# Performance work log

Measured on AMD Instinct MI355X. Metric: run time of the kernel, lower is better.

The kernel has to match this reference:

```python
import jax, jax.numpy as jnp
import numpy as np

B, S, E = 4, 2048, 1024

def setup_inputs() -> dict:
    key = jax.random.key(0)
    ks = jax.random.split(key, 9)
    lim = 1.0 / np.sqrt(E)
    inp = {
        "query": jax.random.normal(ks[0], (B, S, E), dtype=jnp.float32),
        "key": jax.random.normal(ks[1], (B, S, E), dtype=jnp.float32),
        "value": jax.random.normal(ks[2], (B, S, E), dtype=jnp.float32),
        "Wq": jax.random.uniform(ks[3], (E, E), jnp.float32, -lim, lim),
        "bq": jax.random.uniform(ks[4], (E,), jnp.float32, -lim, lim),
        "Wk": jax.random.uniform(ks[5], (E, E), jnp.float32, -lim, lim),
        "bk": jax.random.uniform(ks[6], (E,), jnp.float32, -lim, lim),
        "Wv": jax.random.uniform(ks[7], (E, E), jnp.float32, -lim, lim),
        "bv": jax.random.uniform(ks[8], (E,), jnp.float32, -lim, lim),
    }
    return inp

def reference(query, key, value, Wq, bq, Wk, bk, Wv, bv):
    # Linear layers (torch stores weight as [out,in]; here W is [in,out] used as x @ W)
    q = query @ Wq + bq            # [B,S,E]
    k = key @ Wk + bk              # [B,S,E]
    v = value @ Wv + bv            # [B,S,E]
    inv_scale = jnp.asarray(E, q.dtype) ** 0.5
    scores = jnp.einsum("bse,bte->bst", q, k) / inv_scale  # [B,S,S]
    attn = jax.nn.softmax(scores, axis=-1)
    # dropout_p = 0.0 -> identity
    out = jnp.einsum("bst,bte->bse", attn, v)  # [B,S,E]
    return out
```

## Files before the change

### kernel.cpp

```cpp
#include <hip/hip_runtime.h>
#include <hip/hip_bf16.h>


typedef __bf16 bf16_t;
typedef bf16_t bf16x8 __attribute__((ext_vector_type(8)));
typedef bf16_t bf16x4 __attribute__((ext_vector_type(4)));
typedef float  f32x4  __attribute__((ext_vector_type(4)));

typedef const __attribute__((address_space(1))) unsigned gl_uint;
typedef __attribute__((address_space(3))) unsigned lds_uint;

#define BM 128
#define BN 128
#define BK 64

__device__ __forceinline__ void gload_lds16(const void* g, void* l) {
  __builtin_amdgcn_global_load_lds((gl_uint*)g, (lds_uint*)l, 16, 0, 0);
}

#define VMCNT(N) asm volatile("s_waitcnt vmcnt(" #N ")" ::: "memory")
#define LGKM0()  asm volatile("s_waitcnt lgkmcnt(0)" ::: "memory")

__device__ __forceinline__ void gemm_v3(
    const bf16_t* __restrict__ Ab, const bf16_t* __restrict__ Bb,
    bf16_t* Lb, f32x4 acc[4][4])
{
  const int tid  = threadIdx.x;
  const int lane = tid & 63;
  const int l15  = lane & 15;
  const int quad = lane >> 4;
  const int wid  = tid >> 6;
  const int wr   = wid >> 1;
  const int wcl  = wid & 1;
  const int swz0 = (quad ^ (l15 & 7)) * 8;
  const int swz1 = ((quad + 4) ^ (l15 & 7)) * 8;

  const int r8 = tid >> 3, s8 = tid & 7;
  const size_t gbase = (size_t)r8 * 1024 + (size_t)((s8 ^ (r8 & 7)) * 8);
  const int dbase = tid * 8;

#define SLOTA(s) (Lb + (s) * 24576)
#define SLOTB(s) (Lb + (s) * 24576 + 16384)
#define STAGE6(ktile, slot) { \
    const bf16_t* _A = Ab + (size_t)(ktile) * 64; \
    const bf16_t* _B = Bb + (size_t)(ktile) * 64; \
    bf16_t* _la = SLOTA(slot); bf16_t* _lb = SLOTB(slot); \
    gload_lds16(_A + gbase,                     _la + dbase); \
    gload_lds16(_A + gbase + (size_t)64 * 1024, _la + dbase + 4096); \
    gload_lds16(_A + gbase + (size_t)128 * 1024, _la + dbase + 8192); \
    gload_lds16(_A + gbase + (size_t)192 * 1024, _la + dbase + 12288); \
    gload_lds16(_B + gbase,                     _lb + dbase); \
    gload_lds16(_B + gbase + (size_t)64 * 1024, _lb + dbase + 4096); }

  const int aoff = (wr * 64 + l15) * 64;
  const int boff = (wcl * 64 + l15) * 64;

#define RD(slot, FA, FB) { \
    const bf16_t* _a = SLOTA(slot) + aoff; \
    const bf16_t* _b = SLOTB(slot) + boff; \
    _Pragma("unroll") for (int mi = 0; mi < 4; ++mi) { \
      FA[mi][0] = *(const bf16x8*)(_a + mi * 1024 + swz0); \
      FA[mi][1] = *(const bf16x8*)(_a + mi * 1024 + swz1); } \
    _Pragma("unroll") for (int ni = 0; ni < 4; ++ni) { \
      FB[ni][0] = *(const bf16x8*)(_b + ni * 1024 + swz0); \
      FB[ni][1] = *(const bf16x8*)(_b + ni * 1024 + swz1); } }

#define MFM(FA, FB) \
    _Pragma("unroll") for (int kk = 0; kk < 2; ++kk) \
    _Pragma("unroll") for (int mi = 0; mi < 4; ++mi) \
    _Pragma("unroll") for (int ni = 0; ni < 4; ++ni) \
      acc[mi][ni] = __builtin_amdgcn_mfma_f32_16x16x32_bf16( \
          FA[mi][kk], FB[ni][kk], acc[mi][ni], 0, 0, 0);

  bf16x8 fa0[4][2], fb0[4][2], fa1[4][2], fb1[4][2];

  STAGE6(0, 0); STAGE6(1, 1); STAGE6(2, 2);
  VMCNT(6);
  __builtin_amdgcn_s_barrier();
  RD(0, fa0, fb0);
  LGKM0();
  __builtin_amdgcn_s_barrier();

#pragma unroll
  for (int kt = 0; kt < 14; ++kt) {
    const int ss = kt % 3;
    const int rs = (kt + 1) % 3;
    if (kt <= 12) STAGE6(kt + 3, ss);
    if ((kt & 1) == 0) { RD(rs, fa1, fb1); MFM(fa0, fb0); }
    else               { RD(rs, fa0, fb0); MFM(fa1, fb1); }
    if (kt <= 12) { VMCNT(6); }
    else          { VMCNT(0); }
    __builtin_amdgcn_s_barrier();
  }
  RD(0, fa1, fb1); MFM(fa0, fb0);
  MFM(fa1, fb1);

#undef SLOTA
#undef SLOTB
#undef STAGE6
#undef RD
#undef MFM
}

__global__ __launch_bounds__(512, 2)
void qkv_v3(const bf16_t* __restrict__ qb, const bf16_t* __restrict__ kb,
            const bf16_t* __restrict__ vb, const bf16_t* __restrict__ Wqt,
            const bf16_t* __restrict__ Wkt, const bf16_t* __restrict__ Wvt,
            const float* __restrict__ bq, const float* __restrict__ bk,
            const float* __restrict__ bv, bf16_t* __restrict__ qp,
            bf16_t* __restrict__ kp, bf16_t* __restrict__ vT)
{
  __shared__ __align__(16) bf16_t lds[3 * 24576];
  const int L   = blockIdx.x;
  const int lin = (L & 7) * 96 + (L >> 3);
  const int z   = lin >> 8;
  const int r   = lin & 255;
  const int by  = r >> 3, bx = r & 7;
  const int K = 1024, N = 1024;

  const bf16_t* A    = (z == 0) ? qb : (z == 1) ? kb : vb;
  const bf16_t* W    = (z == 0) ? Wqt : (z == 1) ? Wkt : Wvt;
  const float*  bias = (z == 0) ? bq : (z == 1) ? bk : bv;

  f32x4 acc[4][4];
  const f32x4 z4 = {0.f, 0.f, 0.f, 0.f};
#pragma unroll
  for (int i = 0; i < 4; ++i)
#pragma unroll
    for (int j = 0; j < 4; ++j) acc[i][j] = z4;

  gemm_v3(A + (size_t)by * 256 * K, W + (size_t)bx * 128 * K, lds, acc);

  const int tid = threadIdx.x;
  const int lane = tid & 63, l15 = lane & 15, quad = lane >> 4;
  const int wid = tid >> 6, wr = wid >> 1, wcl = wid & 1;
  const int m0 = by * 256 + wr * 64;
  const int n0 = bx * 128 + wcl * 64;
  float bv_[4];
#pragma unroll
  for (int ni = 0; ni < 4; ++ni) bv_[ni] = bias[n0 + ni * 16 + l15];

  if (z < 2) {
    bf16_t* C = (z == 0) ? qp : kp;
#pragma unroll
    for (int mi = 0; mi < 4; ++mi) {
      const int gm = m0 + mi * 16 + quad * 4;
#pragma unroll
      for (int ni = 0; ni < 4; ++ni) {
        const int gn = n0 + ni * 16 + l15;
        f32x4 a = acc[mi][ni];
#pragma unroll
        for (int rr = 0; rr < 4; ++rr)
          C[(size_t)(gm + rr) * N + gn] = (bf16_t)(a[rr] + bv_[ni]);
      }
    }
  } else {
#pragma unroll
    for (int mi = 0; mi < 4; ++mi) {
      const int gm = m0 + mi * 16 + quad * 4;
      const int b = gm >> 11;
      const int s = gm & 2047;
#pragma unroll
      for (int ni = 0; ni < 4; ++ni) {
        const int gn = n0 + ni * 16 + l15;
        f32x4 a = acc[mi][ni];
        bf16x4 o;
#pragma unroll
        for (int rr = 0; rr < 4; ++rr) o[rr] = (bf16_t)(a[rr] + bv_[ni]);
        *(bf16x4*)&vT[((size_t)b * N + gn) * 2048 + s] = o;
      }
    }
  }
}

__global__ __launch_bounds__(512, 2)
void scores_v3(const bf16_t* __restrict__ qp, const bf16_t* __restrict__ kp,
               bf16_t* __restrict__ P)
{
  __shared__ __align__(16) bf16_t lds[3 * 24576];
  const int L   = blockIdx.x;
  const int lin = (L & 7) * 64 + (L >> 3);
  const int bz  = lin >> 7;
  const int r   = lin & 127;
  const int by  = r >> 4, bx = r & 15;
  const int K = 1024;

  const bf16_t* Ab = qp + (size_t)bz * 2048 * 1024 + (size_t)by * 256 * K;
  const bf16_t* Bb = kp + (size_t)bz * 2048 * 1024 + (size_t)bx * 128 * K;

  f32x4 acc[4][4];
  const f32x4 z4 = {0.f, 0.f, 0.f, 0.f};
#pragma unroll
  for (int i = 0; i < 4; ++i)
#pragma unroll
    for (int j = 0; j < 4; ++j) acc[i][j] = z4;

  gemm_v3(Ab, Bb, lds, acc);

  const int tid = threadIdx.x;
  const int lane = tid & 63, l15 = lane & 15, quad = lane >> 4;
  const int wid = tid >> 6, wr = wid >> 1, wcl = wid & 1;
  const int m0 = by * 256 + wr * 64;
  const int n0 = bx * 128 + wcl * 64;
  bf16_t* C = P + (size_t)bz * 2048 * 2048;
  const float cexp = 0.03125f * 1.4426950408889634f;
#pragma unroll
  for (int mi = 0; mi < 4; ++mi) {
    const int gm = m0 + mi * 16 + quad * 4;
#pragma unroll
    for (int ni = 0; ni < 4; ++ni) {
      const int gn = n0 + ni * 16 + l15;
      f32x4 a = acc[mi][ni];
#pragma unroll
      for (int rr = 0; rr < 4; ++rr)
        C[(size_t)(gm + rr) * 2048 + gn] = (bf16_t)exp2f(a[rr] * cexp);
    }
  }
}

template <bool LSUM>
__device__ __forceinline__ void mfma_tile(const bf16_t* As, const bf16_t* Bs,
                                          f32x4 acc[4][4], f32x4 acc_l[4]) {
  const int lane = threadIdx.x & 63;
  const int quad = lane >> 4;
  const int l15  = lane & 15;
  const int wid  = threadIdx.x >> 6;
  const int wm   = (wid >> 1) * 64;
  const int wn   = (wid & 1) * 64;
  const int csw  = l15 & 7;
  bf16x8 ones;
  if (LSUM) {
#pragma unroll
    for (int t = 0; t < 8; ++t) ones[t] = (bf16_t)1.0f;
  }
#pragma unroll
  for (int ks = 0; ks < 2; ++ks) {
    const int sg = ks * 4 + quad;
    const int c  = (sg ^ csw) * 8;
    bf16x8 fa[4], fb[4];
#pragma unroll
    for (int i = 0; i < 4; ++i)
      fa[i] = *(const bf16x8*)&As[(wm + i * 16 + l15) * BK + c];
#pragma unroll
    for (int i = 0; i < 4; ++i)
      fb[i] = *(const bf16x8*)&Bs[(wn + i * 16 + l15) * BK + c];
#pragma unroll
    for (int mi = 0; mi < 4; ++mi)
#pragma unroll
      for (int ni = 0; ni < 4; ++ni)
        acc[mi][ni] = __builtin_amdgcn_mfma_f32_16x16x32_bf16(
            fa[mi], fb[ni], acc[mi][ni], 0, 0, 0);
    if (LSUM) {
#pragma unroll
      for (int mi = 0; mi < 4; ++mi)
        acc_l[mi] = __builtin_amdgcn_mfma_f32_16x16x32_bf16(
            fa[mi], ones, acc_l[mi], 0, 0, 0);
    }
  }
}

template <bool LSUM>
__device__ __forceinline__ void gemm_core_bf16(
    const bf16_t* __restrict__ Ab, const bf16_t* __restrict__ Bb,
    const int K, bf16_t* As, bf16_t* Bs, f32x4 acc[4][4], f32x4 acc_l[4])
{
  const int tid = threadIdx.x;
  for (int kt = 0; kt < K; kt += BK) {
#pragma unroll
    for (int j = 0; j < 4; ++j) {
      const int lin = j * 256 + tid;
      const int row = lin >> 3;
      const int seg = (lin & 7) ^ (row & 7);
      gload_lds16(Ab + (size_t)row * K + kt + seg * 8, &As[lin * 8]);
    }
#pragma unroll
    for (int j = 0; j < 4; ++j) {
      const int lin = j * 256 + tid;
      const int row = lin >> 3;
      const int seg = (lin & 7) ^ (row & 7);
      gload_lds16(Bb + (size_t)row * K + kt + seg * 8, &Bs[lin * 8]);
    }
    __syncthreads();
    mfma_tile<LSUM>(As, Bs, acc, acc_l);
    __syncthreads();
  }
}

template <int MODE>
__global__ __launch_bounds__(256, 2)
void gemm_att(const bf16_t* __restrict__ A, const bf16_t* __restrict__ Bt,
              void* __restrict__ Cv,
              const int M, const int N, const int K,
              const long long sA, const long long sB, const long long sC)
{
  __shared__ __align__(16) bf16_t As[BM * BK];
  __shared__ __align__(16) bf16_t Bs[BN * BK];

  const int L = blockIdx.x;
  int bx, by, bz;
  if (MODE == 0) {
    const int g = L >> 3;
    const int gst = (L & 7) * 2 + (g >> 6);
    bz = gst >> 2;
    const int s2 = gst & 3;
    const int w = g & 63;
    bx = (s2 & 1) * 8 + (w & 7);
    by = (s2 >> 1) * 8 + (w >> 3);
  } else {
    const int xcd = L & 7;
    const int w = (L >> 3) & 63;
    bz = xcd >> 1;
    bx = w & 7;
    by = (xcd & 1) * 8 + (w >> 3);
  }

  const bf16_t* Ab = A + (size_t)bz * sA + (size_t)by * BM * K;
  const bf16_t* Bb = Bt + (size_t)bz * sB + (size_t)bx * BN * K;

  f32x4 acc[4][4];
  f32x4 acc_l[4];
  const f32x4 z4 = {0.f, 0.f, 0.f, 0.f};
#pragma unroll
  for (int i = 0; i < 4; ++i) {
    acc_l[i] = z4;
#pragma unroll
    for (int j = 0; j < 4; ++j) acc[i][j] = z4;
  }

  gemm_core_bf16<MODE == 1>(Ab, Bb, K, As, Bs, acc, acc_l);

  const int lane = threadIdx.x & 63;
  const int quad = lane >> 4;
  const int l15  = lane & 15;
  const int wid  = threadIdx.x >> 6;
  const int wm = (wid >> 1) * 64, wn = (wid & 1) * 64;
  const int m0 = by * BM, n0 = bx * BN;

  if (MODE == 0) {
    const float cexp = 0.03125f * 1.4426950408889634f;
    bf16_t* C = (bf16_t*)Cv + (size_t)bz * sC;
#pragma unroll
    for (int mi = 0; mi < 4; ++mi) {
      const int gm = m0 + wm + mi * 16 + quad * 4;
#pragma unroll
      for (int ni = 0; ni < 4; ++ni) {
        const int gn = n0 + wn + ni * 16 + l15;
        f32x4 a = acc[mi][ni];
#pragma unroll
        for (int r = 0; r < 4; ++r)
          C[(size_t)(gm + r) * N + gn] = (bf16_t)exp2f(a[r] * cexp);
      }
    }
  } else {
    float* C = (float*)Cv + (size_t)bz * sC;
#pragma unroll
    for (int mi = 0; mi < 4; ++mi) {
      const int gm = m0 + wm + mi * 16 + quad * 4;
      float il[4];
#pragma unroll
      for (int r = 0; r < 4; ++r) il[r] = 1.0f / acc_l[mi][r];
#pragma unroll
      for (int ni = 0; ni < 4; ++ni) {
        const int gn = n0 + wn + ni * 16 + l15;
        f32x4 a = acc[mi][ni];
#pragma unroll
        for (int r = 0; r < 4; ++r)
          C[(size_t)(gm + r) * N + gn] = a[r] * il[r];
      }
    }
  }
}

__global__ __launch_bounds__(256)
void prep(const float* __restrict__ q, const float* __restrict__ k,
          const float* __restrict__ v, const float* __restrict__ Wq,
          const float* __restrict__ Wk, const float* __restrict__ Wv,
          bf16_t* __restrict__ qo, bf16_t* __restrict__ ko,
          bf16_t* __restrict__ vo, bf16_t* __restrict__ Wqt,
          bf16_t* __restrict__ Wkt, bf16_t* __restrict__ Wvt) {
  const int L = blockIdx.x;
  const int tid = threadIdx.x;
  if (L < 24576) {
    const int z = L >> 13;
    const int blk = L & 8191;
    const float* in = (z == 0) ? q : (z == 1) ? k : v;
    bf16_t* out = (z == 0) ? qo : (z == 1) ? ko : vo;
    const size_t i = ((size_t)blk * 256 + tid) * 4;
    const float4 w = *(const float4*)(in + i);
    bf16x4 o;
    o[0] = (bf16_t)w.x; o[1] = (bf16_t)w.y; o[2] = (bf16_t)w.z; o[3] = (bf16_t)w.w;
    *(bf16x4*)(out + i) = o;
  } else {
    const int t = L - 24576;
    const int z = t >> 8;
    const int wi = t & 255;
    const float* W = (z == 0) ? Wq : (z == 1) ? Wk : Wv;
    bf16_t* Wt = (z == 0) ? Wqt : (z == 1) ? Wkt : Wvt;
    __shared__ float tile[64][65];
    const int n0 = (wi & 15) * 64;
    const int k0 = (wi >> 4) * 64;
#pragma unroll
    for (int it = 0; it < 16; ++it) {
      const int idx = it * 256 + tid;
      const int r = idx >> 6, c = idx & 63;
      tile[r][c] = W[(size_t)(k0 + r) * 1024 + n0 + c];
    }
    __syncthreads();
#pragma unroll
    for (int it = 0; it < 16; ++it) {
      const int idx = it * 256 + tid;
      const int r = idx >> 6, c = idx & 63;
      Wt[(size_t)(n0 + r) * 1024 + k0 + c] = (bf16_t)tile[c][r];
    }
  }
}

extern "C" void kernel_launch(void* const* d_in, const int* in_sizes, int n_in,
                              void* d_out, int out_size, void* d_ws, size_t ws_size,
                              hipStream_t stream) {
  const int B = 4, S = 2048, E = 1024;
  const size_t BSE = (size_t)B * S * E;
  const size_t EE  = (size_t)E * E;

  const float* q_in = (const float*)d_in[0];
  const float* k_in = (const float*)d_in[1];
  const float* v_in = (const float*)d_in[2];
  const float* Wq = (const float*)d_in[3];
  const float* bq = (const float*)d_in[4];
  const float* Wk = (const float*)d_in[5];
  const float* bk = (const float*)d_in[6];
  const float* Wv = (const float*)d_in[7];
  const float* bv = (const float*)d_in[8];
  float* out = (float*)d_out;

  char* ws = (char*)d_ws;
  bf16_t* Wqt = (bf16_t*)ws;
  bf16_t* Wkt = Wqt + EE;
  bf16_t* Wvt = Wkt + EE;
  bf16_t* qb  = Wvt + EE;
  bf16_t* kb  = qb + BSE;
  bf16_t* vb  = kb + BSE;
  bf16_t* qp  = vb + BSE;
  bf16_t* kp  = qp + BSE;
  bf16_t* vT  = kp + BSE;
  bf16_t* P   = vT + BSE;

  prep<<<25344, 256, 0, stream>>>(q_in, k_in, v_in, Wq, Wk, Wv,
                                  qb, kb, vb, Wqt, Wkt, Wvt);

  qkv_v3<<<768, 512, 0, stream>>>(qb, kb, vb, Wqt, Wkt, Wvt,
                                  bq, bk, bv, qp, kp, vT);

  scores_v3<<<512, 512, 0, stream>>>(qp, kp, P);

  gemm_att<1><<<512, 256, 0, stream>>>(
      P, vT, out, S, E, S,
      (long long)S * S, (long long)E * S, (long long)S * E);

  (void)in_sizes; (void)n_in; (void)out_size; (void)ws_size;
}
```

Baseline: 284.0 us.

## Move PV GEMM to pipelined 256x128 kernel; revert QKV to simple 128x128 GEMM

The pipelined triple-buffered gemm_v3 core is templated on K stride and tile count, and optionally accumulates row sums via an MFMA against a ones vector. The P·V GEMM now uses it with 256x128 tiles and 512 threads, replacing the single-buffered 128x128 kernel, so load latency is hidden. Meanwhile the QKV projection switches back to the simpler single-buffered 128x128 kernel with 1536 blocks. This trades pipelining in QKV for more blocks there, and gives PV larger tiles but only 256 blocks.

```diff
diff --git a/kernel.cpp b/kernel.cpp
--- a/kernel.cpp
+++ b/kernel.cpp
@@ -21,9 +21,10 @@
 #define VMCNT(N) asm volatile("s_waitcnt vmcnt(" #N ")" ::: "memory")
 #define LGKM0()  asm volatile("s_waitcnt lgkmcnt(0)" ::: "memory")
 
+template <int KS, int NT, bool LSUM>
 __device__ __forceinline__ void gemm_v3(
     const bf16_t* __restrict__ Ab, const bf16_t* __restrict__ Bb,
-    bf16_t* Lb, f32x4 acc[4][4])
+    bf16_t* Lb, f32x4 acc[4][4], f32x4 acc_l[4])
 {
   const int tid  = threadIdx.x;
   const int lane = tid & 63;
@@ -35,8 +36,12 @@
   const int swz0 = (quad ^ (l15 & 7)) * 8;
   const int swz1 = ((quad + 4) ^ (l15 & 7)) * 8;
 
+  bf16x8 ones;
+#pragma unroll
+  for (int t = 0; t < 8; ++t) ones[t] = (bf16_t)1.0f;
+
   const int r8 = tid >> 3, s8 = tid & 7;
-  const size_t gbase = (size_t)r8 * 1024 + (size_t)((s8 ^ (r8 & 7)) * 8);
+  const size_t gbase = (size_t)r8 * KS + (size_t)((s8 ^ (r8 & 7)) * 8);
   const int dbase = tid * 8;
 
 #define SLOTA(s) (Lb + (s) * 24576)
@@ -45,12 +50,12 @@
     const bf16_t* _A = Ab + (size_t)(ktile) * 64; \
     const bf16_t* _B = Bb + (size_t)(ktile) * 64; \
     bf16_t* _la = SLOTA(slot); bf16_t* _lb = SLOTB(slot); \
-    gload_lds16(_A + gbase,                     _la + dbase); \
-    gload_lds16(_A + gbase + (size_t)64 * 1024, _la + dbase + 4096); \
-    gload_lds16(_A + gbase + (size_t)128 * 1024, _la + dbase + 8192); \
-    gload_lds16(_A + gbase + (size_t)192 * 1024, _la + dbase + 12288); \
-    gload_lds16(_B + gbase,                     _lb + dbase); \
-    gload_lds16(_B + gbase + (size_t)64 * 1024, _lb + dbase + 4096); }
+    gload_lds16(_A + gbase,                      _la + dbase); \
+    gload_lds16(_A + gbase + (size_t)64 * KS,    _la + dbase + 4096); \
+    gload_lds16(_A + gbase + (size_t)128 * KS,   _la + dbase + 8192); \
+    gload_lds16(_A + gbase + (size_t)192 * KS,   _la + dbase + 12288); \
+    gload_lds16(_B + gbase,                      _lb + dbase); \
+    gload_lds16(_B + gbase + (size_t)64 * KS,    _lb + dbase + 4096); }
 
   const int aoff = (wr * 64 + l15) * 64;
   const int boff = (wcl * 64 + l15) * 64;
@@ -65,12 +70,16 @@
       FB[ni][0] = *(const bf16x8*)(_b + ni * 1024 + swz0); \
       FB[ni][1] = *(const bf16x8*)(_b + ni * 1024 + swz1); } }
 
-#define MFM(FA, FB) \
-    _Pragma("unroll") for (int kk = 0; kk < 2; ++kk) \
-    _Pragma("unroll") for (int mi = 0; mi < 4; ++mi) \
-    _Pragma("unroll") for (int ni = 0; ni < 4; ++ni) \
-      acc[mi][ni] = __builtin_amdgcn_mfma_f32_16x16x32_bf16( \
-          FA[mi][kk], FB[ni][kk], acc[mi][ni], 0, 0, 0);
+#define MFM(FA, FB) { \
+    _Pragma("unroll") for (int kk = 0; kk < 2; ++kk) { \
+      _Pragma("unroll") for (int mi = 0; mi < 4; ++mi) \
+      _Pragma("unroll") for (int ni = 0; ni < 4; ++ni) \
+        acc[mi][ni] = __builtin_amdgcn_mfma_f32_16x16x32_bf16( \
+            FA[mi][kk], FB[ni][kk], acc[mi][ni], 0, 0, 0); \
+      if constexpr (LSUM) { \
+        _Pragma("unroll") for (int mi = 0; mi < 4; ++mi) \
+          acc_l[mi] = __builtin_amdgcn_mfma_f32_16x16x32_bf16( \
+              FA[mi][kk], ones, acc_l[mi], 0, 0, 0); } } }
 
   bf16x8 fa0[4][2], fb0[4][2], fa1[4][2], fb1[4][2];
 
@@ -82,17 +91,17 @@
   __builtin_amdgcn_s_barrier();
 
 #pragma unroll
-  for (int kt = 0; kt < 14; ++kt) {
+  for (int kt = 0; kt < NT - 2; ++kt) {
     const int ss = kt % 3;
     const int rs = (kt + 1) % 3;
-    if (kt <= 12) STAGE6(kt + 3, ss);
+    if (kt <= NT - 4) STAGE6(kt + 3, ss);
     if ((kt & 1) == 0) { RD(rs, fa1, fb1); MFM(fa0, fb0); }
     else               { RD(rs, fa0, fb0); MFM(fa1, fb1); }
-    if (kt <= 12) { VMCNT(6); }
-    else          { VMCNT(0); }
+    if (kt <= NT - 4) { VMCNT(6); }
+    else              { VMCNT(0); }
     __builtin_amdgcn_s_barrier();
   }
-  RD(0, fa1, fb1); MFM(fa0, fb0);
+  RD((NT - 1) % 3, fa1, fb1); MFM(fa0, fb0);
   MFM(fa1, fb1);
 
 #undef SLOTA
@@ -102,25 +111,87 @@
 #undef MFM
 }
 
-__global__ __launch_bounds__(512, 2)
-void qkv_v3(const bf16_t* __restrict__ qb, const bf16_t* __restrict__ kb,
-            const bf16_t* __restrict__ vb, const bf16_t* __restrict__ Wqt,
-            const bf16_t* __restrict__ Wkt, const bf16_t* __restrict__ Wvt,
-            const float* __restrict__ bq, const float* __restrict__ bk,
-            const float* __restrict__ bv, bf16_t* __restrict__ qp,
-            bf16_t* __restrict__ kp, bf16_t* __restrict__ vT)
+__device__ __forceinline__ void mfma_tile128(const bf16_t* As, const bf16_t* Bs,
+                                             f32x4 acc[4][4]) {
+  const int lane = threadIdx.x & 63;
+  const int quad = lane >> 4;
+  const int l15  = lane & 15;
+  const int wid  = threadIdx.x >> 6;
+  const int wm   = (wid >> 1) * 64;
+  const int wn   = (wid & 1) * 64;
+  const int csw  = l15 & 7;
+#pragma unroll
+  for (int ks = 0; ks < 2; ++ks) {
+    const int sg = ks * 4 + quad;
+    const int c  = (sg ^ csw) * 8;
+    bf16x8 fa[4], fb[4];
+#pragma unroll
+    for (int i = 0; i < 4; ++i)
+      fa[i] = *(const bf16x8*)&As[(wm + i * 16 + l15) * BK + c];
+#pragma unroll
+    for (int i = 0; i < 4; ++i)
+      fb[i] = *(const bf16x8*)&Bs[(wn + i * 16 + l15) * BK + c];
+#pragma unroll
+    for (int mi = 0; mi < 4; ++mi)
+#pragma unroll
+      for (int ni = 0; ni < 4; ++ni)
+        acc[mi][ni] = __builtin_amdgcn_mfma_f32_16x16x32_bf16(
+            fa[mi], fb[ni], acc[mi][ni], 0, 0, 0);
+  }
+}
+
+__device__ __forceinline__ void gemm_core128(
+    const bf16_t* __restrict__ Ab, const bf16_t* __restrict__ Bb,
+    const int K, bf16_t* As, bf16_t* Bs, f32x4 acc[4][4])
 {
-  __shared__ __align__(16) bf16_t lds[3 * 24576];
-  const int L   = blockIdx.x;
-  const int lin = (L & 7) * 96 + (L >> 3);
-  const int z   = lin >> 8;
-  const int r   = lin & 255;
-  const int by  = r >> 3, bx = r & 7;
-  const int K = 1024, N = 1024;
+  const int tid = threadIdx.x;
+  for (int kt = 0; kt < K; kt += BK) {
+#pragma unroll
+    for (int j = 0; j < 4; ++j) {
+      const int lin = j * 256 + tid;
+      const int row = lin >> 3;
+      const int seg = (lin & 7) ^ (row & 7);
+      gload_lds16(Ab + (size_t)row * K + kt + seg * 8, &As[lin * 8]);
+    }
+#pragma unroll
+    for (int j = 0; j < 4; ++j) {
+      const int lin = j * 256 + tid;
+      const int row = lin >> 3;
+      const int seg = (lin & 7) ^ (row & 7);
+      gload_lds16(Bb + (size_t)row * K + kt + seg * 8, &Bs[lin * 8]);
+    }
+    __syncthreads();
+    mfma_tile128(As, Bs, acc);
+    __syncthreads();
+  }
+}
+
+__global__ __launch_bounds__(256, 2)
+void qkv_proj(const bf16_t* __restrict__ qb, const bf16_t* __restrict__ kb,
+              const bf16_t* __restrict__ vb, const bf16_t* __restrict__ Wqt,
+              const bf16_t* __restrict__ Wkt, const bf16_t* __restrict__ Wvt,
+              const float* __restrict__ bq, const float* __restrict__ bk,
+              const float* __restrict__ bv, bf16_t* __restrict__ qp,
+              bf16_t* __restrict__ kp, bf16_t* __restrict__ vT)
+{
+  __shared__ __align__(16) bf16_t As[BM * BK];
+  __shared__ __align__(16) bf16_t Bs[BN * BK];
+
+  const int L = blockIdx.x;
+  const int g = L >> 3;
+  const int gst = (L & 7) * 3 + (g >> 6);
+  const int z  = gst >> 3;
+  const int sy = gst & 7;
+  const int w  = g & 63;
+  const int bx = w & 7;
+  const int by = sy * 8 + (w >> 3);
 
   const bf16_t* A    = (z == 0) ? qb : (z == 1) ? kb : vb;
   const bf16_t* W    = (z == 0) ? Wqt : (z == 1) ? Wkt : Wvt;
   const float*  bias = (z == 0) ? bq : (z == 1) ? bk : bv;
+  const int K = 1024, N = 1024;
+  const bf16_t* Ab = A + (size_t)by * BM * K;
+  const bf16_t* Bb = W + (size_t)bx * BN * K;
 
   f32x4 acc[4][4];
   const f32x4 z4 = {0.f, 0.f, 0.f, 0.f};
@@ -129,44 +200,33 @@
 #pragma unroll
     for (int j = 0; j < 4; ++j) acc[i][j] = z4;
 
-  gemm_v3(A + (size_t)by * 256 * K, W + (size_t)bx * 128 * K, lds, acc);
-
-  const int tid = threadIdx.x;
-  const int lane = tid & 63, l15 = lane & 15, quad = lane >> 4;
-  const int wid = tid >> 6, wr = wid >> 1, wcl = wid & 1;
-  const int m0 = by * 256 + wr * 64;
-  const int n0 = bx * 128 + wcl * 64;
-  float bv_[4];
-#pragma unroll
-  for (int ni = 0; ni < 4; ++ni) bv_[ni] = bias[n0 + ni * 16 + l15];
-
-  if (z < 2) {
-    bf16_t* C = (z == 0) ? qp : kp;
-#pragma unroll
-    for (int mi = 0; mi < 4; ++mi) {
-      const int gm = m0 + mi * 16 + quad * 4;
-#pragma unroll
-      for (int ni = 0; ni < 4; ++ni) {
-        const int gn = n0 + ni * 16 + l15;
-        f32x4 a = acc[mi][ni];
-#pragma unroll
-        for (int rr = 0; rr < 4; ++rr)
-          C[(size_t)(gm + rr) * N + gn] = (bf16_t)(a[rr] + bv_[ni]);
-      }
-    }
-  } else {
-#pragma unroll
-    for (int mi = 0; mi < 4; ++mi) {
-      const int gm = m0 + mi * 16 + quad * 4;
-      const int b = gm >> 11;
-      const int s = gm & 2047;
-#pragma unroll
-      for (int ni = 0; ni < 4; ++ni) {
-        const int gn = n0 + ni * 16 + l15;
-        f32x4 a = acc[mi][ni];
+  gemm_core128(Ab, Bb, K, As, Bs, acc);
+
+  const int lane = threadIdx.x & 63;
+  const int quad = lane >> 4;
+  const int l15  = lane & 15;
+  const int wid  = threadIdx.x >> 6;
+  const int wm = (wid >> 1) * 64, wn = (wid & 1) * 64;
+  const int m0 = by * BM, n0 = bx * BN;
+#pragma unroll
+  for (int mi = 0; mi < 4; ++mi) {
+#pragma unroll
+    for (int ni = 0; ni < 4; ++ni) {
+      const int gn = n0 + wn + ni * 16 + l15;
+      const int gm = m0 + wm + mi * 16 + quad * 4;
+      const float bv_ = bias[gn];
+      f32x4 a = acc[mi][ni];
+      if (z < 2) {
+        bf16_t* C = (z == 0) ? qp : kp;
+#pragma unroll
+        for (int r = 0; r < 4; ++r)
+          C[(size_t)(gm + r) * N + gn] = (bf16_t)(a[r] + bv_);
+      } else {
+        const int b = gm >> 11;
+        const int s = gm & 2047;
         bf16x4 o;
 #pragma unroll
-        for (int rr = 0; rr < 4; ++rr) o[rr] = (bf16_t)(a[rr] + bv_[ni]);
+        for (int r = 0; r < 4; ++r) o[r] = (bf16_t)(a[r] + bv_);
         *(bf16x4*)&vT[((size_t)b * N + gn) * 2048 + s] = o;
       }
     }
@@ -189,13 +249,16 @@
   const bf16_t* Bb = kp + (size_t)bz * 2048 * 1024 + (size_t)bx * 128 * K;
 
   f32x4 acc[4][4];
+  f32x4 acc_l[4];
   const f32x4 z4 = {0.f, 0.f, 0.f, 0.f};
 #pragma unroll
-  for (int i = 0; i < 4; ++i)
+  for (int i = 0; i < 4; ++i) {
+    acc_l[i] = z4;
 #pragma unroll
     for (int j = 0; j < 4; ++j) acc[i][j] = z4;
-
-  gemm_v3(Ab, Bb, lds, acc);
+  }
+
+  gemm_v3<1024, 16, false>(Ab, Bb, lds, acc, acc_l);
 
   const int tid = threadIdx.x;
   const int lane = tid & 63, l15 = lane & 15, quad = lane >> 4;
@@ -218,104 +281,19 @@
   }
 }
 
-template <bool LSUM>
-__device__ __forceinline__ void mfma_tile(const bf16_t* As, const bf16_t* Bs,
-                                          f32x4 acc[4][4], f32x4 acc_l[4]) {
-  const int lane = threadIdx.x & 63;
-  const int quad = lane >> 4;
-  const int l15  = lane & 15;
-  const int wid  = threadIdx.x >> 6;
-  const int wm   = (wid >> 1) * 64;
-  const int wn   = (wid & 1) * 64;
-  const int csw  = l15 & 7;
-  bf16x8 ones;
-  if (LSUM) {
-#pragma unroll
-    for (int t = 0; t < 8; ++t) ones[t] = (bf16_t)1.0f;
-  }
-#pragma unroll
-  for (int ks = 0; ks < 2; ++ks) {
-    const int sg = ks * 4 + quad;
-    const int c  = (sg ^ csw) * 8;
-    bf16x8 fa[4], fb[4];
-#pragma unroll
-    for (int i = 0; i < 4; ++i)
-      fa[i] = *(const bf16x8*)&As[(wm + i * 16 + l15) * BK + c];
-#pragma unroll
-    for (int i = 0; i < 4; ++i)
-      fb[i] = *(const bf16x8*)&Bs[(wn + i * 16 + l15) * BK + c];
-#pragma unroll
-    for (int mi = 0; mi < 4; ++mi)
-#pragma unroll
-      for (int ni = 0; ni < 4; ++ni)
-        acc[mi][ni] = __builtin_amdgcn_mfma_f32_16x16x32_bf16(
-            fa[mi], fb[ni], acc[mi][ni], 0, 0, 0);
-    if (LSUM) {
-#pragma unroll
-      for (int mi = 0; mi < 4; ++mi)
-        acc_l[mi] = __builtin_amdgcn_mfma_f32_16x16x32_bf16(
-            fa[mi], ones, acc_l[mi], 0, 0, 0);
-    }
-  }
-}
-
-template <bool LSUM>
-__device__ __forceinline__ void gemm_core_bf16(
-    const bf16_t* __restrict__ Ab, const bf16_t* __restrict__ Bb,
-    const int K, bf16_t* As, bf16_t* Bs, f32x4 acc[4][4], f32x4 acc_l[4])
+__global__ __launch_bounds__(512, 2)
+void pv_v3(const bf16_t* __restrict__ P, const bf16_t* __restrict__ vT,
+           float* __restrict__ out)
 {
-  const int tid = threadIdx.x;
-  for (int kt = 0; kt < K; kt += BK) {
-#pragma unroll
-    for (int j = 0; j < 4; ++j) {
-      const int lin = j * 256 + tid;
-      const int row = lin >> 3;
-      const int seg = (lin & 7) ^ (row & 7);
-      gload_lds16(Ab + (size_t)row * K + kt + seg * 8, &As[lin * 8]);
-    }
-#pragma unroll
-    for (int j = 0; j < 4; ++j) {
-      const int lin = j * 256 + tid;
-      const int row = lin >> 3;
-      const int seg = (lin & 7) ^ (row & 7);
-      gload_lds16(Bb + (size_t)row * K + kt + seg * 8, &Bs[lin * 8]);
-    }
-    __syncthreads();
-    mfma_tile<LSUM>(As, Bs, acc, acc_l);
-    __syncthreads();
-  }
-}
-
-template <int MODE>
-__global__ __launch_bounds__(256, 2)
-void gemm_att(const bf16_t* __restrict__ A, const bf16_t* __restrict__ Bt,
-              void* __restrict__ Cv,
-              const int M, const int N, const int K,
-              const long long sA, const long long sB, const long long sC)
-{
-  __shared__ __align__(16) bf16_t As[BM * BK];
-  __shared__ __align__(16) bf16_t Bs[BN * BK];
-
-  const int L = blockIdx.x;
-  int bx, by, bz;
-  if (MODE == 0) {
-    const int g = L >> 3;
-    const int gst = (L & 7) * 2 + (g >> 6);
-    bz = gst >> 2;
-    const int s2 = gst & 3;
-    const int w = g & 63;
-    bx = (s2 & 1) * 8 + (w & 7);
-    by = (s2 >> 1) * 8 + (w >> 3);
-  } else {
-    const int xcd = L & 7;
-    const int w = (L >> 3) & 63;
-    bz = xcd >> 1;
-    bx = w & 7;
-    by = (xcd & 1) * 8 + (w >> 3);
-  }
-
-  const bf16_t* Ab = A + (size_t)bz * sA + (size_t)by * BM * K;
-  const bf16_t* Bb = Bt + (size_t)bz * sB + (size_t)bx * BN * K;
+  __shared__ __align__(16) bf16_t lds[3 * 24576];
+  const int L   = blockIdx.x;
+  const int lin = (L & 7) * 32 + (L >> 3);
+  const int bz  = lin >> 6;
+  const int r   = lin & 63;
+  const int by  = r >> 3, bx = r & 7;
+
+  const bf16_t* Ab = P  + (size_t)bz * 2048 * 2048 + (size_t)by * 256 * 2048;
+  const bf16_t* Bb = vT + (size_t)bz * 1024 * 2048 + (size_t)bx * 128 * 2048;
 
   f32x4 acc[4][4];
   f32x4 acc_l[4];
@@ -327,46 +305,27 @@
     for (int j = 0; j < 4; ++j) acc[i][j] = z4;
   }
 
-  gemm_core_bf16<MODE == 1>(Ab, Bb, K, As, Bs, acc, acc_l);
-
-  const int lane = threadIdx.x & 63;
-  const int quad = lane >> 4;
-  const int l15  = lane & 15;
-  const int wid  = threadIdx.x >> 6;
-  const int wm = (wid >> 1) * 64, wn = (wid & 1) * 64;
-  const int m0 = by * BM, n0 = bx * BN;
-
-  if (MODE == 0) {
-    const float cexp = 0.03125f * 1.4426950408889634f;
-    bf16_t* C = (bf16_t*)Cv + (size_t)bz * sC;
-#pragma unroll
-    for (int mi = 0; mi < 4; ++mi) {
-      const int gm = m0 + wm + mi * 16 + quad * 4;
-#pragma unroll
-      for (int ni = 0; ni < 4; ++ni) {
-        const int gn = n0 + wn + ni * 16 + l15;
-        f32x4 a = acc[mi][ni];
-#pragma unroll
-        for (int r = 0; r < 4; ++r)
-          C[(size_t)(gm + r) * N + gn] = (bf16_t)exp2f(a[r] * cexp);
-      }
-    }
-  } else {
-    float* C = (float*)Cv + (size_t)bz * sC;
-#pragma unroll
-    for (int mi = 0; mi < 4; ++mi) {
-      const int gm = m0 + wm + mi * 16 + quad * 4;
-      float il[4];
-#pragma unroll
-      for (int r = 0; r < 4; ++r) il[r] = 1.0f / acc_l[mi][r];
-#pragma unroll
-      for (int ni = 0; ni < 4; ++ni) {
-        const int gn = n0 + wn + ni * 16 + l15;
-        f32x4 a = acc[mi][ni];
-#pragma unroll
-        for (int r = 0; r < 4; ++r)
-          C[(size_t)(gm + r) * N + gn] = a[r] * il[r];
-      }
+  gemm_v3<2048, 32, true>(Ab, Bb, lds, acc, acc_l);
+
+  const int tid = threadIdx.x;
+  const int lane = tid & 63, l15 = lane & 15, quad = lane >> 4;
+  const int wid = tid >> 6, wr = wid >> 1, wcl = wid & 1;
+  const int m0 = by * 256 + wr * 64;
+  const int n0 = bx * 128 + wcl * 64;
+  float* C = out + (size_t)bz * 2048 * 1024;
+#pragma unroll
+  for (int mi = 0; mi < 4; ++mi) {
+    const int gm = m0 + mi * 16 + quad * 4;
+    float il[4];
+#pragma unroll
+    for (int rr = 0; rr < 4; ++rr) il[rr] = 1.0f / acc_l[mi][rr];
+#pragma unroll
+    for (int ni = 0; ni < 4; ++ni) {
+      const int gn = n0 + ni * 16 + l15;
+      f32x4 a = acc[mi][ni];
+#pragma unroll
+      for (int rr = 0; rr < 4; ++rr)
+        C[(size_t)(gm + rr) * 1024 + gn] = a[rr] * il[rr];
     }
   }
 }
@@ -448,14 +407,12 @@
   prep<<<25344, 256, 0, stream>>>(q_in, k_in, v_in, Wq, Wk, Wv,
                                   qb, kb, vb, Wqt, Wkt, Wvt);
 
-  qkv_v3<<<768, 512, 0, stream>>>(qb, kb, vb, Wqt, Wkt, Wvt,
-                                  bq, bk, bv, qp, kp, vT);
+  qkv_proj<<<1536, 256, 0, stream>>>(qb, kb, vb, Wqt, Wkt, Wvt,
+                                     bq, bk, bv, qp, kp, vT);
 
   scores_v3<<<512, 512, 0, stream>>>(qp, kp, P);
 
-  gemm_att<1><<<512, 256, 0, stream>>>(
-      P, vT, out, S, E, S,
-      (long long)S * S, (long long)E * S, (long long)S * E);
+  pv_v3<<<256, 512, 0, stream>>>(P, vT, out);
 
   (void)in_sizes; (void)n_in; (void)out_size; (void)ws_size;
 }
```

Measured after the change: 288.1 us. About the same (+1.5%).
